# Performance work log

Hardware: AMD Instinct MI355X
Metric: run time of the kernel (lower is better)

The kernel has to match this reference:

```python
import jax, jax.numpy as jnp
import numpy as np

EMB = 1024
H = 16
D = EMB // H  # 64
EPS = 1e-5
SM_SCALE = 1.0  # forward default sm_scale=1.0
CAUSAL = True
NEG = -1e30


def _layernorm(t, g, b):
    # LayerNorm over last dim (head_dim), per torch nn.LayerNorm(head_dim)
    m = jnp.mean(t, axis=-1, keepdims=True)
    v = jnp.mean(jnp.square(t - m), axis=-1, keepdims=True)
    return (t - m) * jax.lax.rsqrt(v + EPS) * g + b


def setup_inputs() -> dict:
    key = jax.random.key(0)
    ks = jax.random.split(key, 8)
    N, L = 2, 2048
    x = jax.random.normal(ks[0], (N, L, EMB), dtype=jnp.float32)
    mask = jnp.ones((N, L), dtype=jnp.int32)  # accepted but unused, as in the torch module
    s = 0.02
    Wq = jax.random.normal(ks[1], (EMB, EMB), dtype=jnp.float32) * s
    Wk = jax.random.normal(ks[2], (EMB, EMB), dtype=jnp.float32) * s
    Wv = jax.random.normal(ks[3], (EMB, EMB), dtype=jnp.float32) * s
    Wo = jax.random.normal(ks[4], (EMB, EMB), dtype=jnp.float32) * s
    bo = jnp.zeros((EMB,), dtype=jnp.float32)
    gq = jnp.ones((D,), dtype=jnp.float32)
    bq = jnp.zeros((D,), dtype=jnp.float32)
    gk = jnp.ones((D,), dtype=jnp.float32)
    bk = jnp.zeros((D,), dtype=jnp.float32)
    return {"x": x, "mask": mask, "Wq": Wq, "Wk": Wk, "Wv": Wv,
            "gq": gq, "bq": bq, "gk": gk, "bk": bk, "Wo": Wo, "bo": bo}


def reference(x, mask, Wq, Wk, Wv, gq, bq, gk, bk, Wo, bo):
    N, L, _ = x.shape
    # QKV projections (torch Linear: x @ W.T), split into heads -> [N, H, L, D]
    q = (x @ Wq.T).reshape(N, L, H, D).transpose(0, 2, 1, 3)
    k = (x @ Wk.T).reshape(N, L, H, D).transpose(0, 2, 1, 3)
    v = (x @ Wv.T).reshape(N, L, H, D).transpose(0, 2, 1, 3)
    # fused_q_norm variant: per-head LayerNorm on Q and K (fused into attention kernel)
    q = _layernorm(q, gq, bq)
    k = _layernorm(k, gk, bk)
    scores = jnp.einsum('nhld,nhmd->nhlm', q, k) * SM_SCALE  # [N,H,L,L]
    if CAUSAL:
        causal = jnp.tril(jnp.ones((L, L), dtype=bool))
        scores = jnp.where(causal, scores, NEG)
    attn = jax.nn.softmax(scores, axis=-1)
    out = jnp.einsum('nhlm,nhmd->nhld', attn, v)
    out = out.transpose(0, 2, 1, 3).reshape(N, L, EMB)
    return out @ Wo.T + bo
```

## Files before the change

### kernel.cpp

```cpp
#include <hip/hip_runtime.h>
#include <stdint.h>

typedef unsigned short u16;
typedef u16   u16x4    __attribute__((ext_vector_type(4)));
typedef u16   u16x8    __attribute__((ext_vector_type(8)));
typedef u16x8 u16x8_ma __attribute__((may_alias));
typedef __bf16 bf16x8  __attribute__((ext_vector_type(8)));
typedef float f32x4    __attribute__((ext_vector_type(4)));
typedef f32x4 f32x4_ma __attribute__((may_alias));

#define EMB    1024
#define NHEAD  16
#define HD     64
#define SEQ    2048
#define NBATCH 2
#define ROWS   (NBATCH*SEQ)
#define SATT   72
#define TSTRIDE 132

__device__ __forceinline__ u16 f2b(float f) {
  uint32_t u; __builtin_memcpy(&u, &f, 4);
  u = u + 0x7fffu + ((u >> 16) & 1u);
  return (u16)(u >> 16);
}
__device__ __forceinline__ u16x8 ld8(const u16* p) { return *(const u16x8_ma*)p; }
__device__ __forceinline__ void  st8(u16* p, u16x8 v) { *(u16x8_ma*)p = v; }
__device__ __forceinline__ bf16x8 asbf(u16x8 v) {
  union { u16x8 u; bf16x8 b; } c; c.u = v; return c.b;
}
__device__ __forceinline__ uint32_t cvtpk(float a, float b) {
  uint32_t r;
  asm("v_cvt_pk_bf16_f32 %0, %1, %2" : "=v"(r) : "v"(a), "v"(b));
  return r;
}
__device__ __forceinline__ void async_cp16(const u16* g, u16* l) {
  __builtin_amdgcn_global_load_lds(
      (const __attribute__((address_space(1))) void*)g,
      (__attribute__((address_space(3))) void*)l, 16, 0, 0);
}
__device__ __forceinline__ void xcd_swz(int gx, int gy, int &bx, int &by) {
  int lin = bx + gx * by;
  int q = (gx * gy) >> 3;
  int w = (lin & 7) * q + (lin >> 3);
  bx = w % gx; by = w / gx;
}

__global__ __launch_bounds__(256) void cvt_all(
    const float* __restrict__ x,
    const float* __restrict__ w0, const float* __restrict__ w1,
    const float* __restrict__ w2, const float* __restrict__ w3,
    u16* __restrict__ xd, u16* __restrict__ d0, u16* __restrict__ d1,
    u16* __restrict__ d2, u16* __restrict__ d3)
{
  int bid = blockIdx.x;
  const float* s; u16* d; int off;
  if (bid < 4096) { s = x; d = xd; off = bid; }
  else {
    int t = bid - 4096; int m = t >> 10; off = t & 1023;
    switch (m) {
      case 0: s = w0; d = d0; break;
      case 1: s = w1; d = d1; break;
      case 2: s = w2; d = d2; break;
      default: s = w3; d = d3; break;
    }
  }
  size_t i = ((size_t)off * 256 + threadIdx.x) * 4;
  f32x4 v = *(const f32x4_ma*)(s + i);
  u16x4 o;
  #pragma unroll
  for (int j = 0; j < 4; j++) o[j] = f2b(v[j]);
  *(u16x4*)(d + i) = o;
}

template<int AMODE>
__device__ __forceinline__ void gemm_acc_128x128(
    const u16* __restrict__ A, const u16* __restrict__ B,
    int m0, int n0, u16* As, u16* Bs, f32x4 acc[4][4])
{
  const int tid  = threadIdx.x;
  const int lane = tid & 63;
  const int wave = tid >> 6;
  const int wm   = (wave >> 1) * 64;
  const int wn   = (wave & 1) * 64;
  const int ar   = tid >> 2;
  const int ac   = (tid & 3) * 8;
  const int lm   = lane & 15;
  const int lk   = (lane >> 4) * 8;

  #pragma unroll
  for (int i = 0; i < 4; i++)
    #pragma unroll
    for (int j = 0; j < 4; j++)
      #pragma unroll
      for (int e = 0; e < 4; e++) acc[i][j][e] = 0.f;

  for (int k0 = 0; k0 < EMB; k0 += 64) {
    size_t a0[2], a1[2];
    #pragma unroll
    for (int pnl = 0; pnl < 2; pnl++) {
      int kc = k0 + pnl * 32 + ac;
      if (AMODE == 0) {
        a0[pnl] = (size_t)(m0 + ar)      * EMB + kc;
        a1[pnl] = (size_t)(m0 + ar + 64) * EMB + kc;
      } else {
        int h = kc >> 6, d = kc & 63;
        int r0 = m0 + ar, r1 = m0 + ar + 64;
        a0[pnl] = (((size_t)((r0 >> 11) * NHEAD + h)) * SEQ + (r0 & (SEQ-1))) * HD + d;
        a1[pnl] = (((size_t)((r1 >> 11) * NHEAD + h)) * SEQ + (r1 & (SEQ-1))) * HD + d;
      }
    }
    __syncthreads();
    #pragma unroll
    for (int pnl = 0; pnl < 2; pnl++) {
      const int pb = pnl * 4096;
      async_cp16(A + a0[pnl], As + pb + tid * 8);
      async_cp16(A + a1[pnl], As + pb + (tid + 256) * 8);
      async_cp16(B + (size_t)(n0 + ar)      * EMB + k0 + pnl * 32 + ac, Bs + pb + tid * 8);
      async_cp16(B + (size_t)(n0 + ar + 64) * EMB + k0 + pnl * 32 + ac, Bs + pb + (tid + 256) * 8);
    }
    __syncthreads();

    #pragma unroll
    for (int pnl = 0; pnl < 2; pnl++) {
      const int pb = pnl * 4096;
      bf16x8 af[4], bfr[4];
      #pragma unroll
      for (int i = 0; i < 4; i++)
        af[i] = asbf(ld8(As + pb + (wm + i * 16 + lm) * 32 + lk));
      #pragma unroll
      for (int j = 0; j < 4; j++)
        bfr[j] = asbf(ld8(Bs + pb + (wn + j * 16 + lm) * 32 + lk));
      #pragma unroll
      for (int i = 0; i < 4; i++)
        #pragma unroll
        for (int j = 0; j < 4; j++)
          acc[i][j] = __builtin_amdgcn_mfma_f32_16x16x32_bf16(af[i], bfr[j], acc[i][j], 0, 0, 0);
    }
  }
}

__device__ __forceinline__ void epilogue_scatter_ln(
    f32x4 acc[4][4], u16* dst, int m0, int n0, int head_base, int Hdst,
    const float* g, const float* b, int do_ln)
{
  const int lane = threadIdx.x & 63, wave = threadIdx.x >> 6;
  const int wm = (wave >> 1) * 64, wn = (wave & 1) * 64;
  const int lm = lane & 15, quad = lane >> 4;

  float gv[4], bv[4];
  #pragma unroll
  for (int j = 0; j < 4; j++) { gv[j] = g[j * 16 + lm]; bv[j] = b[j * 16 + lm]; }

  #pragma unroll
  for (int i = 0; i < 4; i++)
    #pragma unroll
    for (int r = 0; r < 4; r++) {
      float val[4];
      #pragma unroll
      for (int j = 0; j < 4; j++) val[j] = acc[i][j][r];
      if (do_ln) {
        float s = val[0] + val[1] + val[2] + val[3];
        #pragma unroll
        for (int o = 8; o >= 1; o >>= 1) s += __shfl_xor(s, o, 64);
        float mean = s * (1.f / 64.f);
        float ss = 0.f;
        #pragma unroll
        for (int j = 0; j < 4; j++) { val[j] -= mean; ss += val[j] * val[j]; }
        #pragma unroll
        for (int o = 8; o >= 1; o >>= 1) ss += __shfl_xor(ss, o, 64);
        float inv = rsqrtf(ss * (1.f / 64.f) + 1e-5f);
        #pragma unroll
        for (int j = 0; j < 4; j++) val[j] = val[j] * inv * gv[j] + bv[j];
      }
      int row = m0 + wm + i * 16 + quad * 4 + r;
      int bn = row >> 11, l = row & (SEQ - 1);
      #pragma unroll
      for (int j = 0; j < 4; j++) {
        int col = n0 + wn + j * 16 + lm;
        int hl = (col >> 6) - head_base, d = col & 63;
        dst[(((size_t)(bn * Hdst + hl)) * SEQ + l) * HD + d] = f2b(val[j]);
      }
    }
}

__device__ __forceinline__ void epilogue_transpose_v(
    f32x4 acc[4][4], u16* dst, int m0, int n0, int Hdst, u16* Ts)
{
  const int tid = threadIdx.x, lane = tid & 63, wave = tid >> 6;
  const int wm = (wave >> 1) * 64;
  const int lm = lane & 15, quad = lane >> 4;
  const int bn = m0 >> 11, l0 = m0 & (SEQ - 1);

  #pragma unroll
  for (int pass = 0; pass < 2; ++pass) {
    __syncthreads();
    if ((wave & 1) == pass) {
      #pragma unroll
      for (int i = 0; i < 4; i++)
        #pragma unroll
        for (int j = 0; j < 4; j++)
          #pragma unroll
          for (int r = 0; r < 4; r++)
            Ts[(j * 16 + lm) * TSTRIDE + wm + i * 16 + quad * 4 + r] =
                f2b(acc[i][j][r]);
    }
    __syncthreads();
    const int hl = (n0 >> 6) + pass;
    u16* base = dst + ((size_t)(bn * Hdst + hl)) * HD * SEQ + l0;
    #pragma unroll
    for (int it = 0; it < 4; ++it) {
      int e = it * 2048 + tid * 8;
      int d = e >> 7, l = e & 127;
      st8(base + (size_t)d * SEQ + l, ld8(Ts + d * TSTRIDE + l));
    }
  }
}

__global__ __launch_bounds__(256) void gemm_qk(
    const u16* __restrict__ x,
    const u16* __restrict__ Wq, const u16* __restrict__ Wk,
    const float* __restrict__ gq, const float* __restrict__ bq,
    const float* __restrict__ gk, const float* __restrict__ bk,
    u16* __restrict__ qd, u16* __restrict__ kb)
{
  __shared__ __align__(16) u16 As[128 * 64];
  __shared__ __align__(16) u16 Bs[128 * 64];
  int bx = blockIdx.x, by = blockIdx.y;
  xcd_swz(8, 32, bx, by);
  const int m0 = by * 128, n0 = bx * 128;
  f32x4 acc[4][4];
  if (blockIdx.z == 0) {
    gemm_acc_128x128<0>(x, Wq, m0, n0, As, Bs, acc);
    epilogue_scatter_ln(acc, qd, m0, n0, 0, NHEAD, gq, bq, 1);
  } else {
    gemm_acc_128x128<0>(x, Wk, m0, n0, As, Bs, acc);
    epilogue_scatter_ln(acc, kb, m0, n0, 0, NHEAD, gk, bk, 1);
  }
}

__global__ __launch_bounds__(256) void gemm_v(
    const u16* __restrict__ x, const u16* __restrict__ Wv,
    u16* __restrict__ vb)
{
  __shared__ __align__(16) u16 buf[128 * 64 * 2];
  u16* As = buf;
  u16* Bs = buf + 128 * 64;
  int bx = blockIdx.x, by = blockIdx.y;
  xcd_swz(8, 32, bx, by);
  const int m0 = by * 128, n0 = bx * 128;
  f32x4 acc[4][4];
  gemm_acc_128x128<0>(x, Wv, m0, n0, As, Bs, acc);
  epilogue_transpose_v(acc, vb, m0, n0, NHEAD, buf);
}

__global__ __launch_bounds__(256) void gemm_q(
    const u16* __restrict__ x, const u16* __restrict__ Wq,
    const float* __restrict__ gq, const float* __restrict__ bq,
    u16* __restrict__ qd)
{
  __shared__ __align__(16) u16 As[128 * 64];
  __shared__ __align__(16) u16 Bs[128 * 64];
  int bx = blockIdx.x, by = blockIdx.y;
  xcd_swz(8, 32, bx, by);
  const int m0 = by * 128, n0 = bx * 128;
  f32x4 acc[4][4];
  gemm_acc_128x128<0>(x, Wq, m0, n0, As, Bs, acc);
  epilogue_scatter_ln(acc, qd, m0, n0, 0, NHEAD, gq, bq, 1);
}
__global__ __launch_bounds__(256) void gemm_kv(
    const u16* __restrict__ x,
    const u16* __restrict__ Wk, const u16* __restrict__ Wv,
    const float* __restrict__ gk, const float* __restrict__ bk,
    u16* __restrict__ k, u16* __restrict__ v, int head_lo, int hpp)
{
  __shared__ __align__(16) u16 buf[128 * 64 * 2];
  u16* As = buf;
  u16* Bs = buf + 128 * 64;
  int bx = blockIdx.x, by = blockIdx.y;
  xcd_swz(hpp / 2, 32, bx, by);
  const int m0 = by * 128, n0 = bx * 128;
  const u16* W = (blockIdx.z == 0 ? Wk : Wv) + (size_t)head_lo * HD * EMB;
  f32x4 acc[4][4];
  gemm_acc_128x128<0>(x, W, m0, n0, As, Bs, acc);
  if (blockIdx.z == 0)
    epilogue_scatter_ln(acc, k, m0, n0, 0, hpp, gk, bk, 1);
  else
    epilogue_transpose_v(acc, v, m0, n0, hpp, buf);
}

__global__ __launch_bounds__(256, 4) void attn(
    u16* qd, const u16* __restrict__ K, const u16* __restrict__ V,
    int head_lo, int hpp)
{
  __shared__ __align__(16) u16 Ks[2][64 * SATT];
  __shared__ __align__(16) u16 Vt[2][64 * SATT];

  const int hl = blockIdx.y, n = blockIdx.z;
  const int perm = (7 * blockIdx.x + (hl & 7) + 8 * n) & 31;
  const int p = perm ^ (31 * (hl >> 3));
  const int tid = threadIdx.x, lane = tid & 63, wave = tid >> 6;
  const int lm = lane & 15, quad = lane >> 4, lk = quad * 8;
  u16* Qh = qd + ((size_t)(n * NHEAD + head_lo + hl)) * SEQ * HD;
  const u16* Kh = K + ((size_t)(n * hpp + hl)) * SEQ * HD;
  const u16* Vh = V + ((size_t)(n * hpp + hl)) * HD * SEQ;

  const int sr = tid >> 3;
  const int sc = (tid & 7) * 8;
  const int vd = tid >> 2;
  const int vc = (tid & 3) * 16;

  bf16x8 aq[2];
  #pragma unroll
  for (int ks = 0; ks < 2; ++ks)
    aq[ks] = asbf(ld8(Qh + (size_t)(p * 64 + wave * 16 + lm) * HD + ks * 32 + lk));

  u16x8 kr0, kr1, vr0, vr1;
  kr0 = ld8(Kh + (size_t)(sr)      * HD + sc);
  kr1 = ld8(Kh + (size_t)(sr + 32) * HD + sc);
  vr0 = ld8(Vh + (size_t)vd * SEQ + vc);
  vr1 = ld8(Vh + (size_t)vd * SEQ + vc + 8);
  st8(&Ks[0][sr * SATT + sc], kr0);
  st8(&Ks[0][(sr + 32) * SATT + sc], kr1);
  st8(&Vt[0][vd * SATT + vc], vr0);
  st8(&Vt[0][vd * SATT + vc + 8], vr1);
  kr0 = ld8(Kh + (size_t)(64 + sr)      * HD + sc);
  kr1 = ld8(Kh + (size_t)(64 + sr + 32) * HD + sc);
  vr0 = ld8(Vh + (size_t)vd * SEQ + 64 + vc);
  vr1 = ld8(Vh + (size_t)vd * SEQ + 64 + vc + 8);
  __syncthreads();

  f32x4 oacc[4];
  #pragma unroll
  for (int j = 0; j < 4; j++)
    #pragma unroll
    for (int e = 0; e < 4; e++) oacc[j][e] = 0.f;
  float m_i = -1e30f, psum = 0.f;

  const int idx0 = (((quad & 1) * 2) * 16 + lm) * 4;
  const int idx1 = idx0 + 64;
  const int qrow = p * 64 + wave * 16 + lm;

  for (int t = 0; t <= p; ++t) {
    const int cur = t & 1;
    if (t < p) {
      const int nb = 1 - cur;
      st8(&Ks[nb][sr * SATT + sc], kr0);
      st8(&Ks[nb][(sr + 32) * SATT + sc], kr1);
      st8(&Vt[nb][vd * SATT + vc], vr0);
      st8(&Vt[nb][vd * SATT + vc + 8], vr1);
      if (t + 1 < p) {
        const size_t base = (size_t)(t + 2) * 64;
        kr0 = ld8(Kh + (base + sr)      * HD + sc);
        kr1 = ld8(Kh + (base + sr + 32) * HD + sc);
        vr0 = ld8(Vh + (size_t)vd * SEQ + base + vc);
        vr1 = ld8(Vh + (size_t)vd * SEQ + base + vc + 8);
      }
    }

    f32x4 s[4];
    #pragma unroll
    for (int j = 0; j < 4; j++)
      #pragma unroll
      for (int e = 0; e < 4; e++) s[j][e] = 0.f;
    __builtin_amdgcn_s_setprio(1);
    #pragma unroll
    for (int ks = 0; ks < 2; ++ks)
      #pragma unroll
      for (int j = 0; j < 4; j++) {
        bf16x8 ak = asbf(ld8(&Ks[cur][(j * 16 + lm) * SATT + ks * 32 + lk]));
        s[j] = __builtin_amdgcn_mfma_f32_16x16x32_bf16(ak, aq[ks], s[j], 0, 0, 0);
      }
    __builtin_amdgcn_s_setprio(0);

    if (t == p) {
      #pragma unroll
      for (int j = 0; j < 4; j++)
        #pragma unroll
        for (int r = 0; r < 4; r++)
          if (t * 64 + j * 16 + quad * 4 + r > qrow) s[j][r] = -1e30f;
    }

    float mx = fmaxf(fmaxf(s[0][0], s[0][1]), fmaxf(s[0][2], s[0][3]));
    #pragma unroll
    for (int j = 1; j < 4; j++)
      mx = fmaxf(mx, fmaxf(fmaxf(s[j][0], s[j][1]), fmaxf(s[j][2], s[j][3])));
    mx = fmaxf(mx, __shfl_xor(mx, 16, 64));
    mx = fmaxf(mx, __shfl_xor(mx, 32, 64));
    const float mnew = fmaxf(m_i, mx);
    const float alpha = __expf(m_i - mnew);
    m_i = mnew;
    float part = 0.f;
    #pragma unroll
    for (int j = 0; j < 4; j++)
      #pragma unroll
      for (int r = 0; r < 4; r++) {
        float pv = __expf(s[j][r] - mnew);
        s[j][r] = pv;
        part += pv;
      }
    psum = psum * alpha + part;

    float ar_[4];
    #pragma unroll
    for (int r = 0; r < 4; r++)
      ar_[r] = __shfl(alpha, (lane & 48) | (quad * 4 + r), 64);
    #pragma unroll
    for (int j = 0; j < 4; j++)
      #pragma unroll
      for (int r = 0; r < 4; r++) oacc[j][r] *= ar_[r];

    uint32_t u[8];
    #pragma unroll
    for (int j = 0; j < 4; j++) {
      u[2 * j]     = cvtpk(s[j][0], s[j][1]);
      u[2 * j + 1] = cvtpk(s[j][2], s[j][3]);
    }

    __builtin_amdgcn_s_setprio(1);
    #pragma unroll
    for (int ks = 0; ks < 2; ++ks) {
      union { uint32_t w[4]; bf16x8 v; } cv;
      #pragma unroll
      for (int w = 0; w < 4; w++) {
        int lo = __builtin_amdgcn_ds_bpermute(w < 2 ? idx0 : idx1,
                                              (int)u[ks * 4 + (w & 1)]);
        int hi = __builtin_amdgcn_ds_bpermute(w < 2 ? idx0 : idx1,
                                              (int)u[ks * 4 + 2 + (w & 1)]);
        cv.w[w] = (quad < 2) ? (uint32_t)lo : (uint32_t)hi;
      }
      bf16x8 ap = cv.v;
      #pragma unroll
      for (int j = 0; j < 4; j++) {
        bf16x8 bv = asbf(ld8(&Vt[cur][(j * 16 + lm) * SATT + ks * 32 + lk]));
        oacc[j] = __builtin_amdgcn_mfma_f32_16x16x32_bf16(ap, bv, oacc[j], 0, 0, 0);
      }
    }
    __builtin_amdgcn_s_setprio(0);
    __syncthreads();
  }

  float s_ = psum;
  s_ += __shfl_xor(s_, 16, 64);
  s_ += __shfl_xor(s_, 32, 64);
  const float inv = 1.0f / s_;
  float ir_[4];
  #pragma unroll
  for (int r = 0; r < 4; r++)
    ir_[r] = __shfl(inv, (lane & 48) | (quad * 4 + r), 64);
  #pragma unroll
  for (int r = 0; r < 4; r++) {
    const int row = p * 64 + wave * 16 + quad * 4 + r;
    #pragma unroll
    for (int j = 0; j < 4; j++)
      Qh[(size_t)row * HD + j * 16 + lm] = f2b(oacc[j][r] * ir_[r]);
  }
}

__global__ __launch_bounds__(256) void gemm_out(
    const u16* __restrict__ ao, const u16* __restrict__ Wo,
    const float* __restrict__ bo, float* __restrict__ out)
{
  __shared__ __align__(16) u16 As[64 * 64];
  __shared__ __align__(16) u16 Bs[128 * 64];
  int bx = blockIdx.x, by = blockIdx.y;
  xcd_swz(8, 64, bx, by);
  const int m0 = by * 64, n0 = bx * 128;
  const int tid  = threadIdx.x;
  const int lane = tid & 63;
  const int wave = tid >> 6;
  const int wm   = (wave >> 1) * 32;
  const int wn   = (wave & 1) * 64;
  const int ar   = tid >> 2;
  const int ac   = (tid & 3) * 8;
  const int lm   = lane & 15;
  const int lk   = (lane >> 4) * 8;

  f32x4 acc[2][4];
  #pragma unroll
  for (int i = 0; i < 2; i++)
    #pragma unroll
    for (int j = 0; j < 4; j++)
      #pragma unroll
      for (int e = 0; e < 4; e++) acc[i][j][e] = 0.f;

  for (int k0 = 0; k0 < EMB; k0 += 64) {
    size_t aoff[2];
    #pragma unroll
    for (int pnl = 0; pnl < 2; pnl++) {
      int kc = k0 + pnl * 32 + ac, h = kc >> 6, d = kc & 63;
      int r0 = m0 + ar;
      aoff[pnl] = (((size_t)((r0 >> 11) * NHEAD + h)) * SEQ + (r0 & (SEQ-1))) * HD + d;
    }
    __syncthreads();
    #pragma unroll
    for (int pnl = 0; pnl < 2; pnl++) {
      async_cp16(ao + aoff[pnl], As + pnl * 2048 + tid * 8);
      async_cp16(Wo + (size_t)(n0 + ar)      * EMB + k0 + pnl * 32 + ac, Bs + pnl * 4096 + tid * 8);
      async_cp16(Wo + (size_t)(n0 + ar + 64) * EMB + k0 + pnl * 32 + ac, Bs + pnl * 4096 + (tid + 256) * 8);
    }
    __syncthreads();

    #pragma unroll
    for (int pnl = 0; pnl < 2; pnl++) {
      bf16x8 af[2], bfr[4];
      #pragma unroll
      for (int i = 0; i < 2; i++)
        af[i] = asbf(ld8(As + pnl * 2048 + (wm + i * 16 + lm) * 32 + lk));
      #pragma unroll
      for (int j = 0; j < 4; j++)
        bfr[j] = asbf(ld8(Bs + pnl * 4096 + (wn + j * 16 + lm) * 32 + lk));
      #pragma unroll
      for (int i = 0; i < 2; i++)
        #pragma unroll
        for (int j = 0; j < 4; j++)
          acc[i][j] = __builtin_amdgcn_mfma_f32_16x16x32_bf16(af[i], bfr[j], acc[i][j], 0, 0, 0);
    }
  }

  const int quad = lane >> 4;
  #pragma unroll
  for (int j = 0; j < 4; j++) {
    int col = n0 + wn + j * 16 + lm;
    float bias = bo[col];
    #pragma unroll
    for (int i = 0; i < 2; i++)
      #pragma unroll
      for (int r = 0; r < 4; r++) {
        int row = m0 + wm + i * 16 + quad * 4 + r;
        out[(size_t)row * EMB + col] = acc[i][j][r] + bias;
      }
  }
}

extern "C" void kernel_launch(void* const* d_in, const int* in_sizes, int n_in,
                              void* d_out, int out_size, void* d_ws, size_t ws_size,
                              hipStream_t stream)
{
  const float* xf  = (const float*)d_in[0];
  const float* Wqf = (const float*)d_in[2];
  const float* Wkf = (const float*)d_in[3];
  const float* Wvf = (const float*)d_in[4];
  const float* gq  = (const float*)d_in[5];
  const float* bq  = (const float*)d_in[6];
  const float* gk  = (const float*)d_in[7];
  const float* bk  = (const float*)d_in[8];
  const float* Wof = (const float*)d_in[9];
  const float* bo  = (const float*)d_in[10];

  const size_t MB = 1u << 20;
  u16* xb  = (u16*)d_ws;
  u16* wqb = xb  + (size_t)ROWS * EMB;
  u16* wkb = wqb + (size_t)EMB * EMB;
  u16* wvb = wkb + (size_t)EMB * EMB;
  u16* wob = wvb + (size_t)EMB * EMB;
  u16* kvbase = wob + (size_t)EMB * EMB;

  size_t avail = (ws_size > 16 * MB) ? ws_size - 16 * MB : 2 * MB;
  int hpp = NHEAD;
  while ((size_t)hpp * MB > avail && hpp > 2) hpp >>= 1;
  const size_t kv_elems = (size_t)hpp * NBATCH * SEQ * HD;
  u16* kbuf = kvbase;
  u16* vbuf = kbuf + kv_elems;

  u16* qd = (u16*)d_in[0];
  float* out = (float*)d_out;

  cvt_all<<<dim3(8192), 256, 0, stream>>>(xf, Wqf, Wkf, Wvf, Wof,
                                          xb, wqb, wkb, wvb, wob);
  if (hpp == NHEAD) {
    gemm_qk<<<dim3(8, 32, 2), 256, 0, stream>>>(xb, wqb, wkb,
                                                gq, bq, gk, bk, qd, kbuf);
    gemm_v<<<dim3(8, 32), 256, 0, stream>>>(xb, wvb, vbuf);
    attn<<<dim3(32, NHEAD, NBATCH), 256, 0, stream>>>(qd, kbuf, vbuf, 0, NHEAD);
  } else {
    gemm_q<<<dim3(8, 32), 256, 0, stream>>>(xb, wqb, gq, bq, qd);
    for (int g = 0; g < NHEAD / hpp; ++g) {
      gemm_kv<<<dim3(hpp / 2, 32, 2), 256, 0, stream>>>(xb, wkb, wvb, gk, bk,
                                                        kbuf, vbuf, g * hpp, hpp);
      attn<<<dim3(32, hpp, NBATCH), 256, 0, stream>>>(qd, kbuf, vbuf, g * hpp, hpp);
    }
  }
  gemm_out<<<dim3(8, 64), 256, 0, stream>>>(qd, wob, bo, out);
}
```

Baseline: 206.0 us.

## Use two waves per attention block with 32 query rows each and XOR-swizzled LDS

The attention kernel now runs 128 threads (2 waves), each wave handling two 16-row query subtiles. Each K and V fragment read from LDS is reused for two MFMAs, which halves LDS read traffic per FLOP. The padded LDS stride is replaced by an XOR swizzle to avoid bank conflicts while shrinking shared memory. In exchange, register pressure roughly doubles for accumulators, there are fewer waves per block to hide latency, and each thread issues more global loads per tile.

Result: slower. 232.4 us (+12.8%).

```diff
diff --git a/kernel.cpp b/kernel.cpp
--- a/kernel.cpp
+++ b/kernel.cpp
@@ -15,7 +15,6 @@
 #define SEQ    2048
 #define NBATCH 2
 #define ROWS   (NBATCH*SEQ)
-#define SATT   72
 #define TSTRIDE 132
 
 __device__ __forceinline__ u16 f2b(float f) {
@@ -43,6 +42,9 @@
   int q = (gx * gy) >> 3;
   int w = (lin & 7) * q + (lin >> 3);
   bx = w % gx; by = w / gx;
+}
+__device__ __forceinline__ int swz(int row, int col) {
+  return row * 64 + (col ^ ((row & 7) << 3));
 }
 
 __global__ __launch_bounds__(256) void cvt_all(
@@ -288,12 +290,12 @@
     epilogue_transpose_v(acc, v, m0, n0, hpp, buf);
 }
 
-__global__ __launch_bounds__(256, 4) void attn(
+__global__ __launch_bounds__(128, 3) void attn(
     u16* qd, const u16* __restrict__ K, const u16* __restrict__ V,
     int head_lo, int hpp)
 {
-  __shared__ __align__(16) u16 Ks[2][64 * SATT];
-  __shared__ __align__(16) u16 Vt[2][64 * SATT];
+  __shared__ __align__(16) u16 Ks[2][64 * 64];
+  __shared__ __align__(16) u16 Vt[2][64 * 64];
 
   const int hl = blockIdx.y, n = blockIdx.z;
   const int perm = (7 * blockIdx.x + (hl & 7) + 8 * n) & 31;
@@ -304,71 +306,79 @@
   const u16* Kh = K + ((size_t)(n * hpp + hl)) * SEQ * HD;
   const u16* Vh = V + ((size_t)(n * hpp + hl)) * HD * SEQ;
 
-  const int sr = tid >> 3;
-  const int sc = (tid & 7) * 8;
-  const int vd = tid >> 2;
-  const int vc = (tid & 3) * 16;
-
-  bf16x8 aq[2];
-  #pragma unroll
-  for (int ks = 0; ks < 2; ++ks)
-    aq[ks] = asbf(ld8(Qh + (size_t)(p * 64 + wave * 16 + lm) * HD + ks * 32 + lk));
-
-  u16x8 kr0, kr1, vr0, vr1;
-  kr0 = ld8(Kh + (size_t)(sr)      * HD + sc);
-  kr1 = ld8(Kh + (size_t)(sr + 32) * HD + sc);
-  vr0 = ld8(Vh + (size_t)vd * SEQ + vc);
-  vr1 = ld8(Vh + (size_t)vd * SEQ + vc + 8);
-  st8(&Ks[0][sr * SATT + sc], kr0);
-  st8(&Ks[0][(sr + 32) * SATT + sc], kr1);
-  st8(&Vt[0][vd * SATT + vc], vr0);
-  st8(&Vt[0][vd * SATT + vc + 8], vr1);
-  kr0 = ld8(Kh + (size_t)(64 + sr)      * HD + sc);
-  kr1 = ld8(Kh + (size_t)(64 + sr + 32) * HD + sc);
-  vr0 = ld8(Vh + (size_t)vd * SEQ + 64 + vc);
-  vr1 = ld8(Vh + (size_t)vd * SEQ + 64 + vc + 8);
+  const int srow = tid >> 3;
+  const int scol = (tid & 7) * 8;
+
+  bf16x8 aqA[2], aqB[2];
+  #pragma unroll
+  for (int ks = 0; ks < 2; ++ks) {
+    aqA[ks] = asbf(ld8(Qh + (size_t)(p * 64 + wave * 32 + lm)      * HD + ks * 32 + lk));
+    aqB[ks] = asbf(ld8(Qh + (size_t)(p * 64 + wave * 32 + 16 + lm) * HD + ks * 32 + lk));
+  }
+
+  u16x8 kr[4], vr[4];
+  #pragma unroll
+  for (int j = 0; j < 4; j++) {
+    int r = srow + 16 * j;
+    kr[j] = ld8(Kh + (size_t)r * HD + scol);
+    vr[j] = ld8(Vh + (size_t)r * SEQ + scol);
+    st8(&Ks[0][swz(r, scol)], kr[j]);
+    st8(&Vt[0][swz(r, scol)], vr[j]);
+  }
+  #pragma unroll
+  for (int j = 0; j < 4; j++) {
+    int r = srow + 16 * j;
+    kr[j] = ld8(Kh + (size_t)(64 + r) * HD + scol);
+    vr[j] = ld8(Vh + (size_t)r * SEQ + 64 + scol);
+  }
   __syncthreads();
 
-  f32x4 oacc[4];
+  f32x4 oA[4], oB[4];
   #pragma unroll
   for (int j = 0; j < 4; j++)
     #pragma unroll
-    for (int e = 0; e < 4; e++) oacc[j][e] = 0.f;
-  float m_i = -1e30f, psum = 0.f;
+    for (int e = 0; e < 4; e++) { oA[j][e] = 0.f; oB[j][e] = 0.f; }
+  float mA = -1e30f, mB = -1e30f, psA = 0.f, psB = 0.f;
 
   const int idx0 = (((quad & 1) * 2) * 16 + lm) * 4;
   const int idx1 = idx0 + 64;
-  const int qrow = p * 64 + wave * 16 + lm;
+  const int qrowA = p * 64 + wave * 32 + lm;
+  const int qrowB = qrowA + 16;
 
   for (int t = 0; t <= p; ++t) {
     const int cur = t & 1;
     if (t < p) {
       const int nb = 1 - cur;
-      st8(&Ks[nb][sr * SATT + sc], kr0);
-      st8(&Ks[nb][(sr + 32) * SATT + sc], kr1);
-      st8(&Vt[nb][vd * SATT + vc], vr0);
-      st8(&Vt[nb][vd * SATT + vc + 8], vr1);
+      #pragma unroll
+      for (int j = 0; j < 4; j++) {
+        int r = srow + 16 * j;
+        st8(&Ks[nb][swz(r, scol)], kr[j]);
+        st8(&Vt[nb][swz(r, scol)], vr[j]);
+      }
       if (t + 1 < p) {
         const size_t base = (size_t)(t + 2) * 64;
-        kr0 = ld8(Kh + (base + sr)      * HD + sc);
-        kr1 = ld8(Kh + (base + sr + 32) * HD + sc);
-        vr0 = ld8(Vh + (size_t)vd * SEQ + base + vc);
-        vr1 = ld8(Vh + (size_t)vd * SEQ + base + vc + 8);
-      }
-    }
-
-    f32x4 s[4];
+        #pragma unroll
+        for (int j = 0; j < 4; j++) {
+          int r = srow + 16 * j;
+          kr[j] = ld8(Kh + (base + r) * HD + scol);
+          vr[j] = ld8(Vh + (size_t)r * SEQ + base + scol);
+        }
+      }
+    }
+
+    f32x4 sA[4], sB[4];
     #pragma unroll
     for (int j = 0; j < 4; j++)
       #pragma unroll
-      for (int e = 0; e < 4; e++) s[j][e] = 0.f;
+      for (int e = 0; e < 4; e++) { sA[j][e] = 0.f; sB[j][e] = 0.f; }
     __builtin_amdgcn_s_setprio(1);
     #pragma unroll
     for (int ks = 0; ks < 2; ++ks)
       #pragma unroll
       for (int j = 0; j < 4; j++) {
-        bf16x8 ak = asbf(ld8(&Ks[cur][(j * 16 + lm) * SATT + ks * 32 + lk]));
-        s[j] = __builtin_amdgcn_mfma_f32_16x16x32_bf16(ak, aq[ks], s[j], 0, 0, 0);
+        bf16x8 ak = asbf(ld8(&Ks[cur][swz(j * 16 + lm, ks * 32 + lk)]));
+        sA[j] = __builtin_amdgcn_mfma_f32_16x16x32_bf16(ak, aqA[ks], sA[j], 0, 0, 0);
+        sB[j] = __builtin_amdgcn_mfma_f32_16x16x32_bf16(ak, aqB[ks], sB[j], 0, 0, 0);
       }
     __builtin_amdgcn_s_setprio(0);
 
@@ -376,83 +386,123 @@
       #pragma unroll
       for (int j = 0; j < 4; j++)
         #pragma unroll
-        for (int r = 0; r < 4; r++)
-          if (t * 64 + j * 16 + quad * 4 + r > qrow) s[j][r] = -1e30f;
-    }
-
-    float mx = fmaxf(fmaxf(s[0][0], s[0][1]), fmaxf(s[0][2], s[0][3]));
-    #pragma unroll
-    for (int j = 1; j < 4; j++)
-      mx = fmaxf(mx, fmaxf(fmaxf(s[j][0], s[j][1]), fmaxf(s[j][2], s[j][3])));
-    mx = fmaxf(mx, __shfl_xor(mx, 16, 64));
-    mx = fmaxf(mx, __shfl_xor(mx, 32, 64));
-    const float mnew = fmaxf(m_i, mx);
-    const float alpha = __expf(m_i - mnew);
-    m_i = mnew;
-    float part = 0.f;
-    #pragma unroll
-    for (int j = 0; j < 4; j++)
-      #pragma unroll
-      for (int r = 0; r < 4; r++) {
-        float pv = __expf(s[j][r] - mnew);
-        s[j][r] = pv;
-        part += pv;
-      }
-    psum = psum * alpha + part;
-
-    float ar_[4];
-    #pragma unroll
-    for (int r = 0; r < 4; r++)
-      ar_[r] = __shfl(alpha, (lane & 48) | (quad * 4 + r), 64);
-    #pragma unroll
-    for (int j = 0; j < 4; j++)
-      #pragma unroll
-      for (int r = 0; r < 4; r++) oacc[j][r] *= ar_[r];
-
-    uint32_t u[8];
-    #pragma unroll
-    for (int j = 0; j < 4; j++) {
-      u[2 * j]     = cvtpk(s[j][0], s[j][1]);
-      u[2 * j + 1] = cvtpk(s[j][2], s[j][3]);
+        for (int r = 0; r < 4; r++) {
+          int key = t * 64 + j * 16 + quad * 4 + r;
+          if (key > qrowA) sA[j][r] = -1e30f;
+          if (key > qrowB) sB[j][r] = -1e30f;
+        }
+    }
+
+    uint32_t uA[8], uB[8];
+    {
+      float mx = fmaxf(fmaxf(sA[0][0], sA[0][1]), fmaxf(sA[0][2], sA[0][3]));
+      #pragma unroll
+      for (int j = 1; j < 4; j++)
+        mx = fmaxf(mx, fmaxf(fmaxf(sA[j][0], sA[j][1]), fmaxf(sA[j][2], sA[j][3])));
+      mx = fmaxf(mx, __shfl_xor(mx, 16, 64));
+      mx = fmaxf(mx, __shfl_xor(mx, 32, 64));
+      const float mnew = fmaxf(mA, mx);
+      const float alpha = __expf(mA - mnew);
+      mA = mnew;
+      float part = 0.f;
+      #pragma unroll
+      for (int j = 0; j < 4; j++)
+        #pragma unroll
+        for (int r = 0; r < 4; r++) {
+          float pv = __expf(sA[j][r] - mnew);
+          sA[j][r] = pv;
+          part += pv;
+        }
+      psA = psA * alpha + part;
+      float ar_[4];
+      #pragma unroll
+      for (int r = 0; r < 4; r++)
+        ar_[r] = __shfl(alpha, (lane & 48) | (quad * 4 + r), 64);
+      #pragma unroll
+      for (int j = 0; j < 4; j++)
+        #pragma unroll
+        for (int r = 0; r < 4; r++) oA[j][r] *= ar_[r];
+      #pragma unroll
+      for (int j = 0; j < 4; j++) {
+        uA[2 * j]     = cvtpk(sA[j][0], sA[j][1]);
+        uA[2 * j + 1] = cvtpk(sA[j][2], sA[j][3]);
+      }
+    }
+    {
+      float mx = fmaxf(fmaxf(sB[0][0], sB[0][1]), fmaxf(sB[0][2], sB[0][3]));
+      #pragma unroll
+      for (int j = 1; j < 4; j++)
+        mx = fmaxf(mx, fmaxf(fmaxf(sB[j][0], sB[j][1]), fmaxf(sB[j][2], sB[j][3])));
+      mx = fmaxf(mx, __shfl_xor(mx, 16, 64));
+      mx = fmaxf(mx, __shfl_xor(mx, 32, 64));
+      const float mnew = fmaxf(mB, mx);
+      const float alpha = __expf(mB - mnew);
+      mB = mnew;
+      float part = 0.f;
+      #pragma unroll
+      for (int j = 0; j < 4; j++)
+        #pragma unroll
+        for (int r = 0; r < 4; r++) {
+          float pv = __expf(sB[j][r] - mnew);
+          sB[j][r] = pv;
+          part += pv;
+        }
+      psB = psB * alpha + part;
+      float ar_[4];
+      #pragma unroll
+      for (int r = 0; r < 4; r++)
+        ar_[r] = __shfl(alpha, (lane & 48) | (quad * 4 + r), 64);
+      #pragma unroll
+      for (int j = 0; j < 4; j++)
+        #pragma unroll
+        for (int r = 0; r < 4; r++) oB[j][r] *= ar_[r];
+      #pragma unroll
+      for (int j = 0; j < 4; j++) {
+        uB[2 * j]     = cvtpk(sB[j][0], sB[j][1]);
+        uB[2 * j + 1] = cvtpk(sB[j][2], sB[j][3]);
+      }
     }
 
     __builtin_amdgcn_s_setprio(1);
     #pragma unroll
     for (int ks = 0; ks < 2; ++ks) {
-      union { uint32_t w[4]; bf16x8 v; } cv;
+      union { uint32_t w[4]; bf16x8 v; } cA, cB;
       #pragma unroll
       for (int w = 0; w < 4; w++) {
-        int lo = __builtin_amdgcn_ds_bpermute(w < 2 ? idx0 : idx1,
-                                              (int)u[ks * 4 + (w & 1)]);
-        int hi = __builtin_amdgcn_ds_bpermute(w < 2 ? idx0 : idx1,
-                                              (int)u[ks * 4 + 2 + (w & 1)]);
-        cv.w[w] = (quad < 2) ? (uint32_t)lo : (uint32_t)hi;
-      }
-      bf16x8 ap = cv.v;
+        int idx = w < 2 ? idx0 : idx1;
+        int loA = __builtin_amdgcn_ds_bpermute(idx, (int)uA[ks * 4 + (w & 1)]);
+        int hiA = __builtin_amdgcn_ds_bpermute(idx, (int)uA[ks * 4 + 2 + (w & 1)]);
+        cA.w[w] = (quad < 2) ? (uint32_t)loA : (uint32_t)hiA;
+        int loB = __builtin_amdgcn_ds_bpermute(idx, (int)uB[ks * 4 + (w & 1)]);
+        int hiB = __builtin_amdgcn_ds_bpermute(idx, (int)uB[ks * 4 + 2 + (w & 1)]);
+        cB.w[w] = (quad < 2) ? (uint32_t)loB : (uint32_t)hiB;
+      }
       #pragma unroll
       for (int j = 0; j < 4; j++) {
-        bf16x8 bv = asbf(ld8(&Vt[cur][(j * 16 + lm) * SATT + ks * 32 + lk]));
-        oacc[j] = __builtin_amdgcn_mfma_f32_16x16x32_bf16(ap, bv, oacc[j], 0, 0, 0);
+        bf16x8 bv = asbf(ld8(&Vt[cur][swz(j * 16 + lm, ks * 32 + lk)]));
+        oA[j] = __builtin_amdgcn_mfma_f32_16x16x32_bf16(cA.v, bv, oA[j], 0, 0, 0);
+        oB[j] = __builtin_amdgcn_mfma_f32_16x16x32_bf16(cB.v, bv, oB[j], 0, 0, 0);
       }
     }
     __builtin_amdgcn_s_setprio(0);
     __syncthreads();
   }
 
-  float s_ = psum;
-  s_ += __shfl_xor(s_, 16, 64);
-  s_ += __shfl_xor(s_, 32, 64);
-  const float inv = 1.0f / s_;
-  float ir_[4];
-  #pragma unroll
-  for (int r = 0; r < 4; r++)
-    ir_[r] = __shfl(inv, (lane & 48) | (quad * 4 + r), 64);
+  float sa = psA, sb = psB;
+  sa += __shfl_xor(sa, 16, 64); sa += __shfl_xor(sa, 32, 64);
+  sb += __shfl_xor(sb, 16, 64); sb += __shfl_xor(sb, 32, 64);
+  const float invA = 1.0f / sa, invB = 1.0f / sb;
   #pragma unroll
   for (int r = 0; r < 4; r++) {
-    const int row = p * 64 + wave * 16 + quad * 4 + r;
-    #pragma unroll
-    for (int j = 0; j < 4; j++)
-      Qh[(size_t)row * HD + j * 16 + lm] = f2b(oacc[j][r] * ir_[r]);
+    float iA = __shfl(invA, (lane & 48) | (quad * 4 + r), 64);
+    float iB = __shfl(invB, (lane & 48) | (quad * 4 + r), 64);
+    const int rowA = p * 64 + wave * 32 + quad * 4 + r;
+    const int rowB = rowA + 16;
+    #pragma unroll
+    for (int j = 0; j < 4; j++) {
+      Qh[(size_t)rowA * HD + j * 16 + lm] = f2b(oA[j][r] * iA);
+      Qh[(size_t)rowB * HD + j * 16 + lm] = f2b(oB[j][r] * iB);
+    }
   }
 }
 
@@ -571,13 +621,13 @@
     gemm_qk<<<dim3(8, 32, 2), 256, 0, stream>>>(xb, wqb, wkb,
                                                 gq, bq, gk, bk, qd, kbuf);
     gemm_v<<<dim3(8, 32), 256, 0, stream>>>(xb, wvb, vbuf);
-    attn<<<dim3(32, NHEAD, NBATCH), 256, 0, stream>>>(qd, kbuf, vbuf, 0, NHEAD);
+    attn<<<dim3(32, NHEAD, NBATCH), 128, 0, stream>>>(qd, kbuf, vbuf, 0, NHEAD);
   } else {
     gemm_q<<<dim3(8, 32), 256, 0, stream>>>(xb, wqb, gq, bq, qd);
     for (int g = 0; g < NHEAD / hpp; ++g) {
       gemm_kv<<<dim3(hpp / 2, 32, 2), 256, 0, stream>>>(xb, wkb, wvb, gk, bk,
                                                         kbuf, vbuf, g * hpp, hpp);
-      attn<<<dim3(32, hpp, NBATCH), 256, 0, stream>>>(qd, kbuf, vbuf, g * hpp, hpp);
+      attn<<<dim3(32, hpp, NBATCH), 128, 0, stream>>>(qd, kbuf, vbuf, g * hpp, hpp);
     }
   }
   gemm_out<<<dim3(8, 64), 256, 0, stream>>>(qd, wob, bo, out);
```
